# Kernel tuning notes

Hardware: AMD Instinct MI355X
Metric: run time of the kernel (lower is better)

## Reference

```python
import jax, jax.numpy as jnp
import numpy as np

N_HEADS = 16

def setup_inputs() -> dict:
    key = jax.random.key(0)
    qkv = jax.random.normal(key, (4, 3072, 2048), dtype=jnp.float32)
    return {"qkv": qkv}

def reference(qkv) -> jnp.ndarray:
    bs, width, length = qkv.shape
    ch = width // (3 * N_HEADS)
    # [bs*H, 3*ch, T] -> split into q, k, v each [bs*H, ch, T]
    qkv_r = qkv.reshape(bs * N_HEADS, 3 * ch, length)
    q, k, v = qkv_r[:, :ch], qkv_r[:, ch:2 * ch], qkv_r[:, 2 * ch:]
    scale = 1.0 / jnp.sqrt(jnp.sqrt(jnp.float32(ch)))
    # scores: [bs*H, T, T]
    weight = jnp.einsum('bct,bcs->bts', q * scale, k * scale)
    weight = jax.nn.softmax(weight.astype(jnp.float32), axis=-1).astype(weight.dtype)
    a = jnp.einsum('bts,bcs->bct', weight, v)  # [bs*H, ch, T]
    return a.reshape(bs, N_HEADS * ch, length)
```

## Files before the change

kernel.cpp:

```cpp
#include <hip/hip_runtime.h>

namespace {

constexpr int D  = 64;
constexpr int T  = 2048;
constexpr int TQ = 64;
constexpr int NT = T / 64;
constexpr float SCL = 0.125f * 1.44269504088896340736f;

constexpr size_t QP_OFF  = (size_t)64 * 32 * 8192;
constexpr size_t WS_NEED = ((size_t)64 * 32 * 8192 + (size_t)64 * 32 * 4096) * 2;

typedef __bf16 bf16x8 __attribute__((ext_vector_type(8)));
typedef float  f32x4  __attribute__((ext_vector_type(4)));
typedef unsigned short u16x4 __attribute__((ext_vector_type(4)));
typedef unsigned short u16x8 __attribute__((ext_vector_type(8)));

__device__ inline unsigned short f2bf(float f) {
    unsigned int u = __builtin_bit_cast(unsigned int, f);
    u += 0x7FFFu + ((u >> 16) & 1u);
    return (unsigned short)(u >> 16);
}

__device__ inline int frag_off(int row, int c0) {
    int g = (c0 >> 3) ^ ((row >> 1) & 7);
    return row * 64 + g * 8;
}

__device__ inline void async_cp16(const void* g, void* l) {
    __builtin_amdgcn_global_load_lds(
        (const __attribute__((address_space(1))) unsigned int*)g,
        (__attribute__((address_space(3))) unsigned int*)l, 16, 0, 0);
}

__global__ __launch_bounds__(256)
void prepass(const float* __restrict__ qkv, unsigned short* __restrict__ ws) {
    const int tile = blockIdx.x, h = blockIdx.y, z = blockIdx.z;
    const int tid = threadIdx.x;
    const float* src = qkv + (size_t)h * 3 * D * T + (size_t)z * D * T + tile * 64;
    __shared__ unsigned short L[4096];

    if (z == 2) {
        unsigned short* dst = ws + (size_t)(h * 32 + tile) * 8192 + 4096;
        #pragma unroll
        for (int half = 0; half < 2; half++) {
            int idx = half * 256 + tid;
            int row = idx >> 3, g = idx & 7;
            int gg  = g ^ ((row >> 1) & 7);
            f32x4 a = *(const f32x4*)(src + (size_t)row * T + gg * 8);
            f32x4 b = *(const f32x4*)(src + (size_t)row * T + gg * 8 + 4);
            u16x8 wv = { f2bf(a[0]), f2bf(a[1]), f2bf(a[2]), f2bf(a[3]),
                         f2bf(b[0]), f2bf(b[1]), f2bf(b[2]), f2bf(b[3]) };
            *(u16x8*)(dst + idx * 8) = wv;
        }
    } else {
        const float m = (z == 0) ? SCL : 1.0f;
        const int c0 = (tid >> 4) * 4, s4 = tid & 15;
        float fr[4][4];
        #pragma unroll
        for (int r = 0; r < 4; r++)
            *(f32x4*)fr[r] = *(const f32x4*)(src + (size_t)(c0 + r) * T + s4 * 4);
        #pragma unroll
        for (int j = 0; j < 4; j++) {
            int trow = s4 * 4 + j;
            u16x4 wv = { f2bf(fr[0][j] * m), f2bf(fr[1][j] * m),
                         f2bf(fr[2][j] * m), f2bf(fr[3][j] * m) };
            *(u16x4*)(L + frag_off(trow, c0) + (c0 & 7)) = wv;
        }
        __syncthreads();
        unsigned short* dst = (z == 0)
            ? ws + QP_OFF + (size_t)(h * 32 + tile) * 4096
            : ws + (size_t)(h * 32 + tile) * 8192;
        #pragma unroll
        for (int i = 0; i < 2; i++)
            *(u16x8*)(dst + tid * 16 + i * 8) =
                *(const u16x8*)(L + tid * 16 + i * 8);
    }
}


#define ATTN_BODY(KT, B)                                                      \
  {                                                                           \
    const int kt_ = (KT);                                                     \
    __syncthreads();   \
    if (kt_ < NT - 1) {                                                       \
      const char* gsrc = kvbase + (size_t)(kt_ + 1) * 16384;                  \
      _Pragma("unroll")                                                       \
      for (int i = 0; i < 4; i++)                                             \
        async_cp16(gsrc + i * 1024, stage[(B) ^ 1] + i * 1024);               \
    }                                                                         \
    f32x4 acc_s[2][2];                                                        \
    _Pragma("unroll")                                                         \
    for (int si = 0; si < 2; si++)                                            \
      _Pragma("unroll")                                                       \
      for (int ti = 0; ti < 2; ti++)                                          \
        acc_s[si][ti] = (f32x4){0.f, 0.f, 0.f, 0.f};                          \
    _Pragma("unroll")                                                         \
    for (int kc = 0; kc < 2; kc++)                                            \
      _Pragma("unroll")                                                       \
      for (int si = 0; si < 2; si++) {                                        \
        bf16x8 aK = *(const bf16x8*)aKp[B][kc][si];                           \
        _Pragma("unroll")                                                     \
        for (int ti = 0; ti < 2; ti++)                                        \
          acc_s[si][ti] = __builtin_amdgcn_mfma_f32_16x16x32_bf16(            \
              aK, bQ[ti][kc], acc_s[si][ti], 0, 0, 0);                        \
      }                                                                       \
                 \
    _Pragma("unroll")                                                         \
    for (int si = 0; si < 2; si++)                                            \
      _Pragma("unroll")                                                       \
      for (int ti = 0; ti < 2; ti++) {                                        \
        float p0 = __builtin_amdgcn_exp2f(acc_s[si][ti][0]);                  \
        float p1 = __builtin_amdgcn_exp2f(acc_s[si][ti][1]);                  \
        float p2 = __builtin_amdgcn_exp2f(acc_s[si][ti][2]);                  \
        float p3 = __builtin_amdgcn_exp2f(acc_s[si][ti][3]);                  \
        l_acc[ti] += (p0 + p1) + (p2 + p3);                                   \
        u16x4 pk = { f2bf(p0), f2bf(p1), f2bf(p2), f2bf(p3) };                \
        *(u16x4*)pwp[si][ti] = pk;                                            \
      }                                                                       \
          \
    bf16x8 bP0 = *(const bf16x8*)bPp[0];                                      \
    bf16x8 bP1 = *(const bf16x8*)bPp[1];                                      \
    _Pragma("unroll")                                                         \
    for (int ci = 0; ci < 4; ci++) {                                          \
      bf16x8 aV = *(const bf16x8*)aVp[B][ci];                                 \
      acc_o[ci][0] = __builtin_amdgcn_mfma_f32_16x16x32_bf16(                 \
          aV, bP0, acc_o[ci][0], 0, 0, 0);                                    \
      acc_o[ci][1] = __builtin_amdgcn_mfma_f32_16x16x32_bf16(                 \
          aV, bP1, acc_o[ci][1], 0, 0, 0);                                    \
    }                                                                         \
  }

__global__ __launch_bounds__(256, 4)
void attn_main(const unsigned short* __restrict__ ws, float* __restrict__ out) {
    const int h  = blockIdx.x;
    const int qt = blockIdx.y;
    const int t0 = qt * TQ;
    const int tid  = threadIdx.x;
    const int lane = tid & 63;
    const int w    = tid >> 6;
    const int sh   = w & 1, th = w >> 1;
    const int ln   = lane & 15, q4 = lane >> 4;

    __shared__ unsigned short KV[2][8192];
    __shared__ unsigned short Ps[4096];

    const unsigned short* qtile = ws + QP_OFF + (size_t)(h * 32 + qt) * 4096;
    bf16x8 bQ[2][2];
    #pragma unroll
    for (int ti = 0; ti < 2; ti++)
        #pragma unroll
        for (int kc = 0; kc < 2; kc++) {
            int t = th * 32 + ti * 16 + ln;
            bQ[ti][kc] = *(const bf16x8*)(qtile + frag_off(t, kc * 32 + q4 * 8));
        }

    const unsigned short* aKp[2][2][2];
    const unsigned short* aVp[2][4];
    const unsigned short* bPp[2];
    unsigned short*       pwp[2][2];
    char*                 stage[2];
    #pragma unroll
    for (int b = 0; b < 2; b++) {
        const unsigned short* Kr = &KV[b][0];
        const unsigned short* Vr = &KV[b][4096];
        #pragma unroll
        for (int kc = 0; kc < 2; kc++)
            #pragma unroll
            for (int si = 0; si < 2; si++)
                aKp[b][kc][si] = Kr + frag_off(sh * 32 + si * 16 + ln, kc * 32 + q4 * 8);
        #pragma unroll
        for (int ci = 0; ci < 4; ci++)
            aVp[b][ci] = Vr + frag_off(ci * 16 + ln, sh * 32 + q4 * 8);
        stage[b] = (char*)&KV[b][0] + w * 4096;
    }
    #pragma unroll
    for (int ti = 0; ti < 2; ti++) {
        bPp[ti] = Ps + frag_off(th * 32 + ti * 16 + ln, sh * 32 + q4 * 8);
        #pragma unroll
        for (int si = 0; si < 2; si++) {
            int t = th * 32 + ti * 16 + ln, c0p = sh * 32 + si * 16 + q4 * 4;
            pwp[si][ti] = Ps + frag_off(t, c0p) + (c0p & 7);
        }
    }

    const char* kvbase = (const char*)ws + (size_t)(h * 32) * 16384
                         + (size_t)w * 4096 + lane * 16;
    #pragma unroll
    for (int i = 0; i < 4; i++) async_cp16(kvbase + i * 1024, stage[0] + i * 1024);

    f32x4 acc_o[4][2];
    #pragma unroll
    for (int ci = 0; ci < 4; ci++)
        #pragma unroll
        for (int ti = 0; ti < 2; ti++) acc_o[ci][ti] = (f32x4){0.f, 0.f, 0.f, 0.f};
    float l_acc[2] = {0.f, 0.f};

    #pragma unroll 1
    for (int m = 0; m < NT / 2; m++) {
        ATTN_BODY(2 * m,     0)
        ATTN_BODY(2 * m + 1, 1)
    }

    __syncthreads();
    float* mrg = (float*)&KV[0][0];
    float* lp  = (float*)Ps;
    #pragma unroll
    for (int ti = 0; ti < 2; ti++) {
        float s = l_acc[ti];
        s += __shfl_xor(s, 16, 64);
        s += __shfl_xor(s, 32, 64);
        if (q4 == 0) lp[th * 64 + sh * 32 + ti * 16 + ln] = s;
    }
    if (sh == 0) {
        float* base = mrg + th * 2048;
        #pragma unroll
        for (int ci = 0; ci < 4; ci++)
            #pragma unroll
            for (int ti = 0; ti < 2; ti++)
                *(f32x4*)(base + (ci * 2 + ti) * 256 + lane * 4) = acc_o[ci][ti];
    }
    __syncthreads();
    if (sh == 1) {
        float* base = mrg + th * 2048;
        float linv[2];
        #pragma unroll
        for (int ti = 0; ti < 2; ti++) {
            int tt = ti * 16 + ln;
            linv[ti] = 1.0f / (lp[th * 64 + tt] + lp[th * 64 + 32 + tt]);
        }
        float* ob = out + (size_t)h * D * T + t0 + th * 32;
        #pragma unroll
        for (int ci = 0; ci < 4; ci++)
            #pragma unroll
            for (int ti = 0; ti < 2; ti++) {
                f32x4 part = *(const f32x4*)(base + (ci * 2 + ti) * 256 + lane * 4);
                #pragma unroll
                for (int r = 0; r < 4; r++) {
                    int c = ci * 16 + q4 * 4 + r;
                    ob[(size_t)c * T + ti * 16 + ln] =
                        (acc_o[ci][ti][r] + part[r]) * linv[ti];
                }
            }
    }
}

__device__ inline bf16x8 frag8(const unsigned short* p, int row, int c0) {
    return *(const bf16x8*)(p + frag_off(row, c0));
}

__global__ __launch_bounds__(256)
void attn_fallback(const float* __restrict__ qkv, float* __restrict__ out) {
    const int h     = blockIdx.y;
    const int t0    = blockIdx.x * TQ;
    const int tid   = threadIdx.x;
    const int lane  = tid & 63;
    const int strip = tid >> 6;
    const int ln    = lane & 15;
    const int q4    = lane >> 4;

    __shared__ unsigned short Qs[TQ * D];
    __shared__ unsigned short Ks[64 * D];
    __shared__ unsigned short Vs[D * 64];
    __shared__ unsigned short Pss[TQ * 64];
    __shared__ float l_lds[TQ];

    const float* qb = qkv + (size_t)h * 3 * D * T;
    const float* kb = qb + (size_t)D * T;
    const float* vb = qb + (size_t)(2 * D) * T;
    const int s4 = tid & 15;
    const int c0 = (tid >> 4) * 4;
    {
        float fr[4][4];
        #pragma unroll
        for (int r = 0; r < 4; r++)
            *(f32x4*)fr[r] = *(const f32x4*)(qb + (size_t)(c0 + r) * T + t0 + s4 * 4);
        #pragma unroll
        for (int j = 0; j < 4; j++) {
            int trow = s4 * 4 + j;
            u16x4 wv = { f2bf(fr[0][j]), f2bf(fr[1][j]), f2bf(fr[2][j]), f2bf(fr[3][j]) };
            *(u16x4*)(Qs + frag_off(trow, c0) + (c0 & 7)) = wv;
        }
    }
    __syncthreads();
    const int arow = strip * 16 + ln;
    const int kg   = q4 * 8;
    const bf16x8 aq0 = frag8(Qs, arow, kg);
    const bf16x8 aq1 = frag8(Qs, arow, 32 + kg);
    f32x4 acc_o[4];
    #pragma unroll
    for (int m = 0; m < 4; m++) acc_o[m] = (f32x4){0.f, 0.f, 0.f, 0.f};
    float l_acc[4] = {0.f, 0.f, 0.f, 0.f};
    constexpr float S2 = 0.125f * 1.44269504088896340736f;
    for (int kt = 0; kt < NT; kt++) {
        const int s0 = kt * 64;
        float kr[4][4], vr[4][4];
        #pragma unroll
        for (int r = 0; r < 4; r++)
            *(f32x4*)kr[r] = *(const f32x4*)(kb + (size_t)(c0 + r) * T + s0 + s4 * 4);
        #pragma unroll
        for (int r = 0; r < 4; r++)
            *(f32x4*)vr[r] = *(const f32x4*)(vb + (size_t)(c0 + r) * T + s0 + s4 * 4);
        __syncthreads();
        #pragma unroll
        for (int j = 0; j < 4; j++) {
            int srow = s4 * 4 + j;
            u16x4 wk = { f2bf(kr[0][j]), f2bf(kr[1][j]), f2bf(kr[2][j]), f2bf(kr[3][j]) };
            *(u16x4*)(Ks + frag_off(srow, c0) + (c0 & 7)) = wk;
        }
        #pragma unroll
        for (int r = 0; r < 4; r++) {
            int row = c0 + r, cc = s4 * 4;
            u16x4 wv = { f2bf(vr[r][0]), f2bf(vr[r][1]), f2bf(vr[r][2]), f2bf(vr[r][3]) };
            *(u16x4*)(Vs + frag_off(row, cc) + (cc & 7)) = wv;
        }
        __syncthreads();
        f32x4 accs[4];
        #pragma unroll
        for (int ns = 0; ns < 4; ns++) {
            bf16x8 b0 = frag8(Ks, ns * 16 + ln, kg);
            bf16x8 b1 = frag8(Ks, ns * 16 + ln, 32 + kg);
            f32x4 z = {0.f, 0.f, 0.f, 0.f};
            z = __builtin_amdgcn_mfma_f32_16x16x32_bf16(aq0, b0, z, 0, 0, 0);
            z = __builtin_amdgcn_mfma_f32_16x16x32_bf16(aq1, b1, z, 0, 0, 0);
            accs[ns] = z;
        }
        #pragma unroll
        for (int ns = 0; ns < 4; ns++) {
            int scol = ns * 16 + ln;
            #pragma unroll
            for (int r = 0; r < 4; r++) {
                float p = __builtin_amdgcn_exp2f(accs[ns][r] * S2);
                l_acc[r] += p;
                int trow = strip * 16 + q4 * 4 + r;
                int g = ((scol >> 3) ^ ((trow >> 1) & 7));
                Pss[trow * 64 + g * 8 + (scol & 7)] = f2bf(p);
            }
        }
        bf16x8 bp0 = frag8(Pss, arow, kg);
        bf16x8 bp1 = frag8(Pss, arow, 32 + kg);
        #pragma unroll
        for (int ms = 0; ms < 4; ms++) {
            bf16x8 av0 = frag8(Vs, ms * 16 + ln, kg);
            bf16x8 av1 = frag8(Vs, ms * 16 + ln, 32 + kg);
            acc_o[ms] = __builtin_amdgcn_mfma_f32_16x16x32_bf16(av0, bp0, acc_o[ms], 0, 0, 0);
            acc_o[ms] = __builtin_amdgcn_mfma_f32_16x16x32_bf16(av1, bp1, acc_o[ms], 0, 0, 0);
        }
    }
    #pragma unroll
    for (int r = 0; r < 4; r++) {
        float s = l_acc[r];
        s += __shfl_xor(s, 1, 64);
        s += __shfl_xor(s, 2, 64);
        s += __shfl_xor(s, 4, 64);
        s += __shfl_xor(s, 8, 64);
        if (ln == 0) l_lds[strip * 16 + q4 * 4 + r] = s;
    }
    const float linv = 1.0f / l_lds[strip * 16 + ln];
    const int tg = t0 + strip * 16 + ln;
    float* ob = out + (size_t)h * D * T;
    #pragma unroll
    for (int ms = 0; ms < 4; ms++)
        #pragma unroll
        for (int r = 0; r < 4; r++) {
            int c = ms * 16 + q4 * 4 + r;
            ob[(size_t)c * T + tg] = acc_o[ms][r] * linv;
        }
}

}

extern "C" void kernel_launch(void* const* d_in, const int* in_sizes, int n_in,
                              void* d_out, int out_size, void* d_ws, size_t ws_size,
                              hipStream_t stream) {
    const float* qkv = (const float*)d_in[0];
    float* out = (float*)d_out;
    if (ws_size >= WS_NEED) {
        prepass<<<dim3(32, 64, 3), 256, 0, stream>>>(qkv, (unsigned short*)d_ws);
        attn_main<<<dim3(64, 32), 256, 0, stream>>>((const unsigned short*)d_ws, out);
    } else {
        attn_fallback<<<dim3(32, 64), 256, 0, stream>>>(qkv, out);
    }
}
```

Baseline: 255.7 us.

## Single-buffer KV tile to raise occupancy and pack bf16 conversions

Removes the double-buffered K/V staging in LDS and replaces it with a single buffer that is loaded and then synchronised before use each iteration. This halves LDS per block and raises the launch-bounds occupancy hint from 4 to 6 blocks per CU. It also switches the P conversion to a packed bf16 convert builtin when one is available. The cost is that the global-to-LDS copy no longer overlaps compute within a block, and each iteration now has an extra barrier, so latency hiding depends on the extra resident blocks.

```diff
diff --git a/kernel.cpp b/kernel.cpp
--- a/kernel.cpp
+++ b/kernel.cpp
@@ -15,11 +15,22 @@
 typedef float  f32x4  __attribute__((ext_vector_type(4)));
 typedef unsigned short u16x4 __attribute__((ext_vector_type(4)));
 typedef unsigned short u16x8 __attribute__((ext_vector_type(8)));
+typedef unsigned int   u32x2 __attribute__((ext_vector_type(2)));
 
 __device__ inline unsigned short f2bf(float f) {
     unsigned int u = __builtin_bit_cast(unsigned int, f);
     u += 0x7FFFu + ((u >> 16) & 1u);
     return (unsigned short)(u >> 16);
+}
+
+__device__ inline unsigned int pkbf(float a, float b) {
+#if __has_builtin(__builtin_amdgcn_cvt_pk_bf16_f32)
+    auto r = __builtin_amdgcn_cvt_pk_bf16_f32(a, b);
+    static_assert(sizeof(r) == 4, "cvt_pk_bf16 size");
+    return __builtin_bit_cast(unsigned int, r);
+#else
+    return (unsigned int)f2bf(a) | ((unsigned int)f2bf(b) << 16);
+#endif
 }
 
 __device__ inline int frag_off(int row, int c0) {
@@ -78,60 +89,7 @@
     }
 }
 
-
-#define ATTN_BODY(KT, B)                                                      \
-  {                                                                           \
-    const int kt_ = (KT);                                                     \
-    __syncthreads();   \
-    if (kt_ < NT - 1) {                                                       \
-      const char* gsrc = kvbase + (size_t)(kt_ + 1) * 16384;                  \
-      _Pragma("unroll")                                                       \
-      for (int i = 0; i < 4; i++)                                             \
-        async_cp16(gsrc + i * 1024, stage[(B) ^ 1] + i * 1024);               \
-    }                                                                         \
-    f32x4 acc_s[2][2];                                                        \
-    _Pragma("unroll")                                                         \
-    for (int si = 0; si < 2; si++)                                            \
-      _Pragma("unroll")                                                       \
-      for (int ti = 0; ti < 2; ti++)                                          \
-        acc_s[si][ti] = (f32x4){0.f, 0.f, 0.f, 0.f};                          \
-    _Pragma("unroll")                                                         \
-    for (int kc = 0; kc < 2; kc++)                                            \
-      _Pragma("unroll")                                                       \
-      for (int si = 0; si < 2; si++) {                                        \
-        bf16x8 aK = *(const bf16x8*)aKp[B][kc][si];                           \
-        _Pragma("unroll")                                                     \
-        for (int ti = 0; ti < 2; ti++)                                        \
-          acc_s[si][ti] = __builtin_amdgcn_mfma_f32_16x16x32_bf16(            \
-              aK, bQ[ti][kc], acc_s[si][ti], 0, 0, 0);                        \
-      }                                                                       \
-                 \
-    _Pragma("unroll")                                                         \
-    for (int si = 0; si < 2; si++)                                            \
-      _Pragma("unroll")                                                       \
-      for (int ti = 0; ti < 2; ti++) {                                        \
-        float p0 = __builtin_amdgcn_exp2f(acc_s[si][ti][0]);                  \
-        float p1 = __builtin_amdgcn_exp2f(acc_s[si][ti][1]);                  \
-        float p2 = __builtin_amdgcn_exp2f(acc_s[si][ti][2]);                  \
-        float p3 = __builtin_amdgcn_exp2f(acc_s[si][ti][3]);                  \
-        l_acc[ti] += (p0 + p1) + (p2 + p3);                                   \
-        u16x4 pk = { f2bf(p0), f2bf(p1), f2bf(p2), f2bf(p3) };                \
-        *(u16x4*)pwp[si][ti] = pk;                                            \
-      }                                                                       \
-          \
-    bf16x8 bP0 = *(const bf16x8*)bPp[0];                                      \
-    bf16x8 bP1 = *(const bf16x8*)bPp[1];                                      \
-    _Pragma("unroll")                                                         \
-    for (int ci = 0; ci < 4; ci++) {                                          \
-      bf16x8 aV = *(const bf16x8*)aVp[B][ci];                                 \
-      acc_o[ci][0] = __builtin_amdgcn_mfma_f32_16x16x32_bf16(                 \
-          aV, bP0, acc_o[ci][0], 0, 0, 0);                                    \
-      acc_o[ci][1] = __builtin_amdgcn_mfma_f32_16x16x32_bf16(                 \
-          aV, bP1, acc_o[ci][1], 0, 0, 0);                                    \
-    }                                                                         \
-  }
-
-__global__ __launch_bounds__(256, 4)
+__global__ __launch_bounds__(256, 6)
 void attn_main(const unsigned short* __restrict__ ws, float* __restrict__ out) {
     const int h  = blockIdx.x;
     const int qt = blockIdx.y;
@@ -142,7 +100,7 @@
     const int sh   = w & 1, th = w >> 1;
     const int ln   = lane & 15, q4 = lane >> 4;
 
-    __shared__ unsigned short KV[2][8192];
+    __shared__ unsigned short KV[8192];
     __shared__ unsigned short Ps[4096];
 
     const unsigned short* qtile = ws + QP_OFF + (size_t)(h * 32 + qt) * 4096;
@@ -155,39 +113,34 @@
             bQ[ti][kc] = *(const bf16x8*)(qtile + frag_off(t, kc * 32 + q4 * 8));
         }
 
-    const unsigned short* aKp[2][2][2];
-    const unsigned short* aVp[2][4];
+    const unsigned short* aKp[2][2];
+    const unsigned short* aVp[4];
     const unsigned short* bPp[2];
-    unsigned short*       pwp[2][2];
-    char*                 stage[2];
-    #pragma unroll
-    for (int b = 0; b < 2; b++) {
-        const unsigned short* Kr = &KV[b][0];
-        const unsigned short* Vr = &KV[b][4096];
+    unsigned int*         pwp[2][2];
+    {
+        const unsigned short* Kr = &KV[0];
+        const unsigned short* Vr = &KV[4096];
         #pragma unroll
         for (int kc = 0; kc < 2; kc++)
             #pragma unroll
             for (int si = 0; si < 2; si++)
-                aKp[b][kc][si] = Kr + frag_off(sh * 32 + si * 16 + ln, kc * 32 + q4 * 8);
+                aKp[kc][si] = Kr + frag_off(sh * 32 + si * 16 + ln, kc * 32 + q4 * 8);
         #pragma unroll
         for (int ci = 0; ci < 4; ci++)
-            aVp[b][ci] = Vr + frag_off(ci * 16 + ln, sh * 32 + q4 * 8);
-        stage[b] = (char*)&KV[b][0] + w * 4096;
-    }
-    #pragma unroll
-    for (int ti = 0; ti < 2; ti++) {
-        bPp[ti] = Ps + frag_off(th * 32 + ti * 16 + ln, sh * 32 + q4 * 8);
-        #pragma unroll
-        for (int si = 0; si < 2; si++) {
-            int t = th * 32 + ti * 16 + ln, c0p = sh * 32 + si * 16 + q4 * 4;
-            pwp[si][ti] = Ps + frag_off(t, c0p) + (c0p & 7);
-        }
-    }
-
+            aVp[ci] = Vr + frag_off(ci * 16 + ln, sh * 32 + q4 * 8);
+        #pragma unroll
+        for (int ti = 0; ti < 2; ti++) {
+            bPp[ti] = Ps + frag_off(th * 32 + ti * 16 + ln, sh * 32 + q4 * 8);
+            #pragma unroll
+            for (int si = 0; si < 2; si++) {
+                int t = th * 32 + ti * 16 + ln, c0p = sh * 32 + si * 16 + q4 * 4;
+                pwp[si][ti] = (unsigned int*)(Ps + frag_off(t, c0p) + (c0p & 7));
+            }
+        }
+    }
+    char* stage = (char*)&KV[0] + w * 4096;
     const char* kvbase = (const char*)ws + (size_t)(h * 32) * 16384
                          + (size_t)w * 4096 + lane * 16;
-    #pragma unroll
-    for (int i = 0; i < 4; i++) async_cp16(kvbase + i * 1024, stage[0] + i * 1024);
 
     f32x4 acc_o[4][2];
     #pragma unroll
@@ -197,13 +150,58 @@
     float l_acc[2] = {0.f, 0.f};
 
     #pragma unroll 1
-    for (int m = 0; m < NT / 2; m++) {
-        ATTN_BODY(2 * m,     0)
-        ATTN_BODY(2 * m + 1, 1)
+    for (int kt = 0; kt < NT; kt++) {
+        __syncthreads();
+        {
+            const char* gsrc = kvbase + (size_t)kt * 16384;
+            #pragma unroll
+            for (int i = 0; i < 4; i++) async_cp16(gsrc + i * 1024, stage + i * 1024);
+        }
+        __syncthreads();
+
+        f32x4 acc_s[2][2];
+        #pragma unroll
+        for (int si = 0; si < 2; si++)
+            #pragma unroll
+            for (int ti = 0; ti < 2; ti++) acc_s[si][ti] = (f32x4){0.f, 0.f, 0.f, 0.f};
+        #pragma unroll
+        for (int kc = 0; kc < 2; kc++)
+            #pragma unroll
+            for (int si = 0; si < 2; si++) {
+                bf16x8 aK = *(const bf16x8*)aKp[kc][si];
+                #pragma unroll
+                for (int ti = 0; ti < 2; ti++)
+                    acc_s[si][ti] = __builtin_amdgcn_mfma_f32_16x16x32_bf16(
+                        aK, bQ[ti][kc], acc_s[si][ti], 0, 0, 0);
+            }
+
+        #pragma unroll
+        for (int si = 0; si < 2; si++)
+            #pragma unroll
+            for (int ti = 0; ti < 2; ti++) {
+                float p0 = __builtin_amdgcn_exp2f(acc_s[si][ti][0]);
+                float p1 = __builtin_amdgcn_exp2f(acc_s[si][ti][1]);
+                float p2 = __builtin_amdgcn_exp2f(acc_s[si][ti][2]);
+                float p3 = __builtin_amdgcn_exp2f(acc_s[si][ti][3]);
+                l_acc[ti] += (p0 + p1) + (p2 + p3);
+                u32x2 pk = { pkbf(p0, p1), pkbf(p2, p3) };
+                *(u32x2*)pwp[si][ti] = pk;
+            }
+
+        bf16x8 bP0 = *(const bf16x8*)bPp[0];
+        bf16x8 bP1 = *(const bf16x8*)bPp[1];
+        #pragma unroll
+        for (int ci = 0; ci < 4; ci++) {
+            bf16x8 aV = *(const bf16x8*)aVp[ci];
+            acc_o[ci][0] = __builtin_amdgcn_mfma_f32_16x16x32_bf16(
+                aV, bP0, acc_o[ci][0], 0, 0, 0);
+            acc_o[ci][1] = __builtin_amdgcn_mfma_f32_16x16x32_bf16(
+                aV, bP1, acc_o[ci][1], 0, 0, 0);
+        }
     }
 
     __syncthreads();
-    float* mrg = (float*)&KV[0][0];
+    float* mrg = (float*)&KV[0];
     float* lp  = (float*)Ps;
     #pragma unroll
     for (int ti = 0; ti < 2; ti++) {
```

New measurement: 279.2 us. 1.09x slower.

## Software-pipeline attention loop: split K/V staging and overlap QK^T with previous PV

Applied to the files above, without the earlier changes.

Splits the shared K/V double buffer into separate K and V buffers that are prefetched at different times. K runs one tile ahead of V, so the QK^T MFMAs for tile j+1 are issued alongside the PV MFMAs for tile j. A prologue and epilogue handle the first and last tiles. The bf16 conversion of P now uses the packed cvt_pk_bf16_f32 builtin when it is available. The aim is to hide LDS and exp latency behind MFMA work and cut conversion ALU cost, at the price of more live registers and more complex control flow.

```diff
diff --git a/kernel.cpp b/kernel.cpp
--- a/kernel.cpp
+++ b/kernel.cpp
@@ -15,11 +15,22 @@
 typedef float  f32x4  __attribute__((ext_vector_type(4)));
 typedef unsigned short u16x4 __attribute__((ext_vector_type(4)));
 typedef unsigned short u16x8 __attribute__((ext_vector_type(8)));
+typedef unsigned int   u32x2 __attribute__((ext_vector_type(2)));
 
 __device__ inline unsigned short f2bf(float f) {
     unsigned int u = __builtin_bit_cast(unsigned int, f);
     u += 0x7FFFu + ((u >> 16) & 1u);
     return (unsigned short)(u >> 16);
+}
+
+__device__ inline unsigned int pkbf(float a, float b) {
+#if __has_builtin(__builtin_amdgcn_cvt_pk_bf16_f32)
+    auto r = __builtin_amdgcn_cvt_pk_bf16_f32(a, b);
+    static_assert(sizeof(r) == 4, "cvt_pk_bf16 size");
+    return __builtin_bit_cast(unsigned int, r);
+#else
+    return (unsigned int)f2bf(a) | ((unsigned int)f2bf(b) << 16);
+#endif
 }
 
 __device__ inline int frag_off(int row, int c0) {
@@ -73,39 +84,52 @@
             : ws + (size_t)(h * 32 + tile) * 8192;
         #pragma unroll
         for (int i = 0; i < 2; i++)
-            *(u16x8*)(dst + tid * 16 + i * 8) =
-                *(const u16x8*)(L + tid * 16 + i * 8);
-    }
-}
-
-
-#define ATTN_BODY(KT, B)                                                      \
-  {                                                                           \
-    const int kt_ = (KT);                                                     \
-    __syncthreads();   \
-    if (kt_ < NT - 1) {                                                       \
-      const char* gsrc = kvbase + (size_t)(kt_ + 1) * 16384;                  \
-      _Pragma("unroll")                                                       \
-      for (int i = 0; i < 4; i++)                                             \
-        async_cp16(gsrc + i * 1024, stage[(B) ^ 1] + i * 1024);               \
-    }                                                                         \
+            *(u16x8*)(dst + tid * 16 + i * 8) = *(const u16x8*)(L + tid * 16 + i * 8);
+    }
+}
+
+
+#define STAGE_K(J, B)                                                         \
+  { const char* g = kvb + (size_t)(J) * 16384;                                \
+    async_cp16(g,        kst[B]);                                             \
+    async_cp16(g + 1024, kst[B] + 1024); }
+#define STAGE_V(J, B)                                                         \
+  { const char* g = kvb + (size_t)(J) * 16384 + 8192;                         \
+    async_cp16(g,        vst[B]);                                             \
+    async_cp16(g + 1024, vst[B] + 1024); }
+
+#define S_PHASE(B)                                                            \
     f32x4 acc_s[2][2];                                                        \
     _Pragma("unroll")                                                         \
-    for (int si = 0; si < 2; si++)                                            \
+    for (int si = 0; si < 2; si++) {                                          \
+      bf16x8 aK0 = *(const bf16x8*)aKp[B][0][si];                             \
       _Pragma("unroll")                                                       \
       for (int ti = 0; ti < 2; ti++)                                          \
-        acc_s[si][ti] = (f32x4){0.f, 0.f, 0.f, 0.f};                          \
+        acc_s[si][ti] = __builtin_amdgcn_mfma_f32_16x16x32_bf16(              \
+            aK0, bQ[ti][0], ZF, 0, 0, 0);                                     \
+    }                                                                         \
     _Pragma("unroll")                                                         \
-    for (int kc = 0; kc < 2; kc++)                                            \
+    for (int si = 0; si < 2; si++) {                                          \
+      bf16x8 aK1 = *(const bf16x8*)aKp[B][1][si];                             \
       _Pragma("unroll")                                                       \
-      for (int si = 0; si < 2; si++) {                                        \
-        bf16x8 aK = *(const bf16x8*)aKp[B][kc][si];                           \
-        _Pragma("unroll")                                                     \
-        for (int ti = 0; ti < 2; ti++)                                        \
-          acc_s[si][ti] = __builtin_amdgcn_mfma_f32_16x16x32_bf16(            \
-              aK, bQ[ti][kc], acc_s[si][ti], 0, 0, 0);                        \
-      }                                                                       \
-                 \
+      for (int ti = 0; ti < 2; ti++)                                          \
+        acc_s[si][ti] = __builtin_amdgcn_mfma_f32_16x16x32_bf16(              \
+            aK1, bQ[ti][1], acc_s[si][ti], 0, 0, 0);                          \
+    }
+
+#define PV_PHASE(VB)                                                          \
+    { bf16x8 bP0 = *(const bf16x8*)bPp[0];                                    \
+      bf16x8 bP1 = *(const bf16x8*)bPp[1];                                    \
+      _Pragma("unroll")                                                       \
+      for (int ci = 0; ci < 4; ci++) {                                        \
+        bf16x8 aV = *(const bf16x8*)aVp[VB][ci];                              \
+        acc_o[ci][0] = __builtin_amdgcn_mfma_f32_16x16x32_bf16(               \
+            aV, bP0, acc_o[ci][0], 0, 0, 0);                                  \
+        acc_o[ci][1] = __builtin_amdgcn_mfma_f32_16x16x32_bf16(               \
+            aV, bP1, acc_o[ci][1], 0, 0, 0);                                  \
+      } }
+
+#define EXP_P()                                                               \
     _Pragma("unroll")                                                         \
     for (int si = 0; si < 2; si++)                                            \
       _Pragma("unroll")                                                       \
@@ -115,21 +139,9 @@
         float p2 = __builtin_amdgcn_exp2f(acc_s[si][ti][2]);                  \
         float p3 = __builtin_amdgcn_exp2f(acc_s[si][ti][3]);                  \
         l_acc[ti] += (p0 + p1) + (p2 + p3);                                   \
-        u16x4 pk = { f2bf(p0), f2bf(p1), f2bf(p2), f2bf(p3) };                \
-        *(u16x4*)pwp[si][ti] = pk;                                            \
-      }                                                                       \
-          \
-    bf16x8 bP0 = *(const bf16x8*)bPp[0];                                      \
-    bf16x8 bP1 = *(const bf16x8*)bPp[1];                                      \
-    _Pragma("unroll")                                                         \
-    for (int ci = 0; ci < 4; ci++) {                                          \
-      bf16x8 aV = *(const bf16x8*)aVp[B][ci];                                 \
-      acc_o[ci][0] = __builtin_amdgcn_mfma_f32_16x16x32_bf16(                 \
-          aV, bP0, acc_o[ci][0], 0, 0, 0);                                    \
-      acc_o[ci][1] = __builtin_amdgcn_mfma_f32_16x16x32_bf16(                 \
-          aV, bP1, acc_o[ci][1], 0, 0, 0);                                    \
-    }                                                                         \
-  }
+        u32x2 pk = { pkbf(p0, p1), pkbf(p2, p3) };                            \
+        *(u32x2*)pwp[si][ti] = pk;                                            \
+      }
 
 __global__ __launch_bounds__(256, 4)
 void attn_main(const unsigned short* __restrict__ ws, float* __restrict__ out) {
@@ -142,7 +154,8 @@
     const int sh   = w & 1, th = w >> 1;
     const int ln   = lane & 15, q4 = lane >> 4;
 
-    __shared__ unsigned short KV[2][8192];
+    __shared__ unsigned short Kb[2][4096];
+    __shared__ unsigned short Vb[2][4096];
     __shared__ unsigned short Ps[4096];
 
     const unsigned short* qtile = ws + QP_OFF + (size_t)(h * 32 + qt) * 4096;
@@ -158,21 +171,20 @@
     const unsigned short* aKp[2][2][2];
     const unsigned short* aVp[2][4];
     const unsigned short* bPp[2];
-    unsigned short*       pwp[2][2];
-    char*                 stage[2];
+    unsigned int*         pwp[2][2];
+    char *kst[2], *vst[2];
     #pragma unroll
     for (int b = 0; b < 2; b++) {
-        const unsigned short* Kr = &KV[b][0];
-        const unsigned short* Vr = &KV[b][4096];
         #pragma unroll
         for (int kc = 0; kc < 2; kc++)
             #pragma unroll
             for (int si = 0; si < 2; si++)
-                aKp[b][kc][si] = Kr + frag_off(sh * 32 + si * 16 + ln, kc * 32 + q4 * 8);
+                aKp[b][kc][si] = &Kb[b][0] + frag_off(sh * 32 + si * 16 + ln, kc * 32 + q4 * 8);
         #pragma unroll
         for (int ci = 0; ci < 4; ci++)
-            aVp[b][ci] = Vr + frag_off(ci * 16 + ln, sh * 32 + q4 * 8);
-        stage[b] = (char*)&KV[b][0] + w * 4096;
+            aVp[b][ci] = &Vb[b][0] + frag_off(ci * 16 + ln, sh * 32 + q4 * 8);
+        kst[b] = (char*)&Kb[b][0] + w * 2048;
+        vst[b] = (char*)&Vb[b][0] + w * 2048;
     }
     #pragma unroll
     for (int ti = 0; ti < 2; ti++) {
@@ -180,30 +192,59 @@
         #pragma unroll
         for (int si = 0; si < 2; si++) {
             int t = th * 32 + ti * 16 + ln, c0p = sh * 32 + si * 16 + q4 * 4;
-            pwp[si][ti] = Ps + frag_off(t, c0p) + (c0p & 7);
-        }
-    }
-
-    const char* kvbase = (const char*)ws + (size_t)(h * 32) * 16384
-                         + (size_t)w * 4096 + lane * 16;
-    #pragma unroll
-    for (int i = 0; i < 4; i++) async_cp16(kvbase + i * 1024, stage[0] + i * 1024);
+            pwp[si][ti] = (unsigned int*)(Ps + frag_off(t, c0p) + (c0p & 7));
+        }
+    }
+    const char* kvb = (const char*)ws + (size_t)(h * 32) * 16384
+                      + (size_t)w * 2048 + lane * 16;
+    const f32x4 ZF = {0.f, 0.f, 0.f, 0.f};
 
     f32x4 acc_o[4][2];
     #pragma unroll
     for (int ci = 0; ci < 4; ci++)
         #pragma unroll
-        for (int ti = 0; ti < 2; ti++) acc_o[ci][ti] = (f32x4){0.f, 0.f, 0.f, 0.f};
+        for (int ti = 0; ti < 2; ti++) acc_o[ci][ti] = ZF;
     float l_acc[2] = {0.f, 0.f};
 
+    STAGE_K(0, 0)
+    __syncthreads();
+    STAGE_K(1, 1) STAGE_V(0, 0)
+    {
+        S_PHASE(0)
+        EXP_P()
+    }
+
     #pragma unroll 1
-    for (int m = 0; m < NT / 2; m++) {
-        ATTN_BODY(2 * m,     0)
-        ATTN_BODY(2 * m + 1, 1)
-    }
-
+    for (int m = 0; m < 15; m++) {
+        const int j = 2 * m + 1;
+        {
+            __syncthreads();
+            STAGE_K(j + 1, 0) STAGE_V(j, 1)
+            S_PHASE(1)
+            PV_PHASE(0)
+            EXP_P()
+        }
+        {
+            __syncthreads();
+            STAGE_K(j + 2, 1) STAGE_V(j + 1, 0)
+            S_PHASE(0)
+            PV_PHASE(1)
+            EXP_P()
+        }
+    }
+
+    {
+        __syncthreads();
+        STAGE_V(31, 1)
+        S_PHASE(1)
+        PV_PHASE(0)
+        EXP_P()
+    }
     __syncthreads();
-    float* mrg = (float*)&KV[0][0];
+    PV_PHASE(1)
+
+    __syncthreads();
+    float* mrg = (float*)&Kb[0][0];
     float* lp  = (float*)Ps;
     #pragma unroll
     for (int ti = 0; ti < 2; ti++) {
```

Measured after the change: 257.9 us. About the same (+0.9%).
